# Kernel tuning notes

Hardware: AMD Instinct MI355X
Metric: run time of the kernel (lower is better)

## Reference

```python
import jax, jax.numpy as jnp
import numpy as np

N_GT, N_NODES, N_SPECIES, N_EDGES, D, L = 512, 399, 200, 397, 64, 2


def setup_inputs() -> dict:
    rng = np.random.default_rng(0)
    # Random recursive trees: parent of node i is uniform in [0, i).
    par = (rng.random((N_GT, N_NODES - 1)) * np.arange(1, N_NODES)).astype(np.int64)
    child = np.broadcast_to(np.arange(1, N_NODES), (N_GT, N_NODES - 1))
    off = (np.arange(N_GT, dtype=np.int64) * N_NODES)[:, None]
    c = (child + off).ravel()
    p = (par + off).ravel()
    # Both directions, as in the original [2, 2E_gt] convention.
    edge_index = np.stack([np.concatenate([c, p]), np.concatenate([p, c])])
    sp = np.full(N_NODES, -1, dtype=np.int64)
    sp[:N_SPECIES] = np.arange(N_SPECIES)
    sp_ids = np.tile(sp, N_GT)
    leaf_mask = sp_ids >= 0
    batch_vec = np.repeat(np.arange(N_GT, dtype=np.int64), N_NODES)
    # Clades: random species subsets per species-tree edge, guaranteed nonempty.
    pe = rng.uniform(0.05, 0.5, (N_EDGES, 1))
    clade_mask = rng.random((N_EDGES, N_SPECIES)) < pe
    clade_mask[np.arange(N_EDGES), rng.integers(0, N_SPECIES, N_EDGES)] = True
    key = jax.random.key(0)
    ks = jax.random.split(key, 3)
    s = 1.0 / np.sqrt(D)
    return {
        "edge_index": jnp.asarray(edge_index),
        "sp_ids": jnp.asarray(sp_ids),
        "leaf_mask": jnp.asarray(leaf_mask),
        "batch_vec": jnp.asarray(batch_vec),
        "clade_mask": jnp.asarray(clade_mask),
        "n_gt": N_GT,
        "emb_table": jax.random.normal(ks[0], (N_SPECIES + 1, D), jnp.float32),
        "W1": jax.random.normal(ks[1], (L, D, D), jnp.float32) * s,
        "b1": jnp.zeros((L, D), jnp.float32),
        "W2": jax.random.normal(ks[2], (L, D, D), jnp.float32) * s,
        "b2": jnp.zeros((L, D), jnp.float32),
        "eps": jnp.zeros((L,), jnp.float32),  # GINConv train_eps init 0
        "ln_gamma": jnp.ones((L, D), jnp.float32),
        "ln_beta": jnp.zeros((L, D), jnp.float32),
    }


def _layernorm(x, g, b):
    mu = x.mean(-1, keepdims=True)
    var = ((x - mu) ** 2).mean(-1, keepdims=True)
    return (x - mu) * jax.lax.rsqrt(var + 1e-5) * g + b


def reference(edge_index, sp_ids, leaf_mask, batch_vec, clade_mask, n_gt,
              emb_table, W1, b1, W2, b2, eps, ln_gamma, ln_beta):
    n_nodes = sp_ids.shape[0]
    n_edges, n_species = clade_mask.shape
    d = emb_table.shape[1]
    # Species embedding (internal nodes -> extra row n_species).
    emb_ids = jnp.where(sp_ids < 0, n_species, sp_ids)
    x = emb_table[emb_ids]  # [Nn, D]
    src, dst = edge_index[0], edge_index[1]
    for l in range(W1.shape[0]):
        # GINConv: mlp((1+eps)*x + sum_neighbors x_j), residual, LayerNorm.
        msg = jax.ops.segment_sum(x[src], dst, num_segments=n_nodes)
        h = (1.0 + eps[l]) * x + msg
        h = jax.nn.relu(h @ W1[l] + b1[l]) @ W2[l] + b2[l]
        x = _layernorm(x + h, ln_gamma[l], ln_beta[l])
        # dropout is identity in eval mode
    # Species pooling: mean over valid leaves per (gene tree, species).
    w = (leaf_mask & (sp_ids >= 0)).astype(x.dtype)  # [Nn]
    comp = batch_vec * n_species + jnp.maximum(sp_ids, 0)
    pool_size = n_gt * n_species
    sums = jax.ops.segment_sum(x * w[:, None], comp, num_segments=pool_size)
    cnts = jax.ops.segment_sum(w, comp, num_segments=pool_size)
    pool = (sums / jnp.maximum(cnts, 1.0)[:, None]).reshape(n_gt, n_species, d)
    valid = (cnts > 0).astype(x.dtype).reshape(n_gt, n_species)  # [G, S]
    # Clade pooling per species-tree edge (vectorized over the per-edge loop).
    mf = clade_mask.astype(x.dtype)  # [E, S]
    csum = jnp.einsum('es,gsd->egd', mf, pool * valid[:, :, None])  # [E,G,D]
    ccnt = mf @ valid.T  # [E, G] valid-species count per (edge, gene tree)
    gt_means = csum / jnp.maximum(ccnt, 1.0)[:, :, None]
    has = (ccnt > 0).astype(x.dtype)  # gene trees with data for this edge
    n_v = has.sum(1)  # [E]
    mean = (gt_means * has[:, :, None]).sum(1) / jnp.maximum(n_v, 1.0)[:, None]
    diff = (gt_means - mean[:, None, :]) * has[:, :, None]
    var = (diff ** 2).sum(1) / jnp.maximum(n_v - 1.0, 1.0)[:, None]  # unbiased
    ok = (n_v > 1)[:, None]
    std = jnp.where(ok, jnp.sqrt(jnp.where(ok, var, 1.0)), 0.0)
    mean = jnp.where((n_v > 0)[:, None], mean, 0.0)
    return jnp.concatenate([mean, std], axis=-1)  # [n_edges, 2*D]
```

## Files before the change

### kernel.cpp

```cpp
#include <hip/hip_runtime.h>

#define SMAX 200
#define NPG 399

typedef __bf16 bf16x8 __attribute__((ext_vector_type(8)));
typedef _Float16 half8 __attribute__((ext_vector_type(8)));
typedef float f32x4 __attribute__((ext_vector_type(4)));

__device__ __forceinline__ unsigned short f2bf(float f) {
  unsigned u = __float_as_uint(f);
  unsigned r = (u + 0x7FFFu + ((u >> 16) & 1u)) >> 16;
  return (unsigned short)r;
}
__device__ __forceinline__ int xel(int node, int dim) {
  return node * 64 + ((((dim >> 3)) ^ (node & 7)) << 3) + (dim & 7);
}

__global__ __launch_bounds__(256) void k_prep(const int* __restrict__ clade,
                                              unsigned short* __restrict__ mfA,
                                              unsigned* __restrict__ mfbits,
                                              int n_edges, int n_species) {
  int stride = gridDim.x * 256;
  for (int idx = blockIdx.x * 256 + threadIdx.x; idx < 25 * 7 * 512;
       idx += stride) {
    int fi = idx >> 9, within = idx & 511;
    int mt = fi / 7, kt = fi % 7;
    int l = within >> 3, j = within & 7;
    int e = mt * 16 + (l & 15);
    int s = kt * 32 + ((l >> 4) & 3) * 8 + j;
    unsigned short v = 0;
    if (e < n_edges && s < n_species && clade[(size_t)e * n_species + s] != 0)
      v = 0x3F80;
    mfA[idx] = v;
  }
  for (int idx = blockIdx.x * 256 + threadIdx.x; idx < 400 * 8; idx += stride) {
    int e = idx >> 3, w = idx & 7;
    unsigned bits = 0;
    if (e < n_edges && w < 7) {
      for (int b = 0; b < 32; ++b) {
        int s = w * 32 + b;
        if (s < n_species && clade[(size_t)e * n_species + s] != 0)
          bits |= 1u << b;
      }
    }
    mfbits[idx] = bits;
  }
}

__global__ __launch_bounds__(512) void k_tree(
    const float* __restrict__ emb, const int* __restrict__ sp,
    const int* __restrict__ leaf, const int* __restrict__ src,
    const int* __restrict__ dst, const float* __restrict__ W1,
    const float* __restrict__ b1, const float* __restrict__ W2,
    const float* __restrict__ b2, const float* __restrict__ eps_p,
    const float* __restrict__ gam, const float* __restrict__ bet,
    const unsigned short* __restrict__ mfA, const unsigned* __restrict__ mfbits,
    _Float16* __restrict__ gmat, float* __restrict__ has, int npg,
    int n_species, int n_edges, int n_gt) {
  __shared__ __attribute__((aligned(16))) _Float16 sA[NPG * 64];
  __shared__ __attribute__((aligned(16))) _Float16 sB[NPG * 64];
  __shared__ __attribute__((aligned(16))) _Float16 sWf[2][2][4096];
  __shared__ __attribute__((aligned(16))) _Float16 sT[8][1024];
  __shared__ int sStart[NPG + 1];
  __shared__ int sChild[NPG - 1];
  __shared__ int sPar[NPG];
  __shared__ int sCnt[NPG];

  int g = blockIdx.x, tid = threadIdx.x;
  int base = g * npg, nEt = npg - 1, ebase = g * nEt;
  int w = tid >> 6, lane = tid & 63;
  int cc = lane & 15, gq = lane >> 4;

  for (int i = tid; i < npg + 1; i += 512) sStart[i] = 0;
  for (int i = tid; i < npg; i += 512) sCnt[i] = 0;
  __syncthreads();
  for (int idx = tid; idx < 4096; idx += 512) {
    int k = idx >> 6, n = idx & 63;
    int frag = (k >> 5) * 4 + (n >> 4);
    int ln = ((k >> 3) & 3) * 16 + (n & 15);
    int j = k & 7;
    int o = frag * 512 + ln * 8 + j;
    sWf[0][0][o] = (_Float16)W1[idx];
    sWf[0][1][o] = (_Float16)W2[idx];
    sWf[1][0][o] = (_Float16)W1[4096 + idx];
    sWf[1][1][o] = (_Float16)W2[4096 + idx];
  }
  for (int idx = tid; idx < npg * 8; idx += 512) {
    int node = idx >> 3, ch = idx & 7;
    int s = sp[base + node];
    int row = (s < 0) ? n_species : s;
    float4 v0 = reinterpret_cast<const float4*>(emb)[row * 16 + ch * 2];
    float4 v1 = reinterpret_cast<const float4*>(emb)[row * 16 + ch * 2 + 1];
    half8 h;
    h[0] = (_Float16)v0.x; h[1] = (_Float16)v0.y;
    h[2] = (_Float16)v0.z; h[3] = (_Float16)v0.w;
    h[4] = (_Float16)v1.x; h[5] = (_Float16)v1.y;
    h[6] = (_Float16)v1.z; h[7] = (_Float16)v1.w;
    *reinterpret_cast<half8*>(&sA[node * 64 + ((ch ^ (node & 7)) << 3)]) = h;
  }
  for (int i = tid; i < nEt; i += 512) {
    int c = src[ebase + i] - base;
    int p = dst[ebase + i] - base;
    sPar[c] = p;
    atomicAdd(&sStart[p + 1], 1);
  }
  __syncthreads();
  if (w == 0) {
    int run = 0;
    for (int chunk = 0; chunk * 64 < npg + 1; ++chunk) {
      int idx = chunk * 64 + lane;
      int v = (idx < npg + 1) ? sStart[idx] : 0;
      for (int off = 1; off < 64; off <<= 1) {
        int t2 = __shfl_up(v, off);
        if (lane >= off) v += t2;
      }
      v += run;
      if (idx < npg + 1) sStart[idx] = v;
      run = __shfl(v, 63);
    }
  }
  __syncthreads();
  for (int c = tid + 1; c < npg; c += 512) {
    int p = sPar[c];
    int pos = sStart[p] + atomicAdd(&sCnt[p], 1);
    sChild[pos] = c;
  }
  __syncthreads();

  _Float16* tb = sT[w];
  int t0w = w * 3;
  int t1w = (w == 7) ? 25 : t0w + 3;
  for (int l = 0; l < 2; ++l) {
    const _Float16* xin = l ? sB : sA;
    _Float16* xout = l ? sA : sB;
    const half8* xin8 = reinterpret_cast<const half8*>(xin);
    float e1 = 1.0f + eps_p[l];
    float b1v[4], b2v[4], gv[4], bv[4];
#pragma unroll
    for (int nt = 0; nt < 4; ++nt) {
      b1v[nt] = b1[l * 64 + cc + 16 * nt];
      b2v[nt] = b2[l * 64 + cc + 16 * nt];
      gv[nt] = gam[l * 64 + cc + 16 * nt];
      bv[nt] = bet[l * 64 + cc + 16 * nt];
    }
    const half8* B1 = reinterpret_cast<const half8*>(sWf[l][0]);
    const half8* B2 = reinterpret_cast<const half8*>(sWf[l][1]);
    for (int t = t0w; t < t1w; ++t) {
      int n0 = t * 16;
      int node = n0 + cc;
      bool vn = node < npg;
      int nd2 = vn ? node : 0;
      int j0v = vn ? sStart[nd2] : 0;
      int cnt = vn ? (sStart[nd2 + 1] - j0v) : 0;
      half8 s0 = xin8[nd2 * 8 + (gq ^ (nd2 & 7))];
      half8 s1 = xin8[nd2 * 8 + ((4 + gq) ^ (nd2 & 7))];
      bool hasp = vn && node > 0;
      int pr = hasp ? sPar[nd2] : 0;
      half8 p0 = xin8[pr * 8 + (gq ^ (pr & 7))];
      half8 p1 = xin8[pr * 8 + ((4 + gq) ^ (pr & 7))];
      float a0f[8], a1f[8];
#pragma unroll
      for (int d = 0; d < 8; ++d) {
        a0f[d] = e1 * (float)s0[d] + (hasp ? (float)p0[d] : 0.f);
        a1f[d] = e1 * (float)s1[d] + (hasp ? (float)p1[d] : 0.f);
      }
      int cmax = cnt;
#pragma unroll
      for (int off = 1; off < 64; off <<= 1)
        cmax = max(cmax, __shfl_xor(cmax, off));
      cmax = __builtin_amdgcn_readfirstlane(cmax);
#pragma unroll 2
      for (int k = 0; k < cmax; ++k) {
        bool act = k < cnt;
        int jidx = act ? (j0v + k) : 0;
        int c = sChild[jidx];
        half8 v0 = xin8[c * 8 + (gq ^ (c & 7))];
        half8 v1 = xin8[c * 8 + ((4 + gq) ^ (c & 7))];
        if (act) {
#pragma unroll
          for (int d = 0; d < 8; ++d) {
            a0f[d] += (float)v0[d];
            a1f[d] += (float)v1[d];
          }
        }
      }
      half8 a0, a1;
#pragma unroll
      for (int d = 0; d < 8; ++d) {
        a0[d] = (_Float16)a0f[d];
        a1[d] = (_Float16)a1f[d];
      }
      f32x4 tacc[4];
#pragma unroll
      for (int nt = 0; nt < 4; ++nt) tacc[nt] = (f32x4){0.f, 0.f, 0.f, 0.f};
#pragma unroll
      for (int nt = 0; nt < 4; ++nt) {
        tacc[nt] = __builtin_amdgcn_mfma_f32_16x16x32_f16(
            a0, B1[nt * 64 + lane], tacc[nt], 0, 0, 0);
        tacc[nt] = __builtin_amdgcn_mfma_f32_16x16x32_f16(
            a1, B1[(4 + nt) * 64 + lane], tacc[nt], 0, 0, 0);
      }
#pragma unroll
      for (int nt = 0; nt < 4; ++nt)
#pragma unroll
        for (int r = 0; r < 4; ++r) {
          int m = gq * 4 + r;
          tb[m * 64 + ((cc + 16 * nt) ^ ((m & 7) << 3))] =
              (_Float16)fmaxf(tacc[nt][r] + b1v[nt], 0.f);
        }
      int sw = (cc & 7) << 3;
      half8 c0 =
          *reinterpret_cast<const half8*>(&tb[cc * 64 + ((gq * 8) ^ sw)]);
      half8 c1 =
          *reinterpret_cast<const half8*>(&tb[cc * 64 + ((32 + gq * 8) ^ sw)]);
      f32x4 hacc[4];
#pragma unroll
      for (int nt = 0; nt < 4; ++nt) hacc[nt] = (f32x4){0.f, 0.f, 0.f, 0.f};
#pragma unroll
      for (int nt = 0; nt < 4; ++nt) {
        hacc[nt] = __builtin_amdgcn_mfma_f32_16x16x32_f16(
            c0, B2[nt * 64 + lane], hacc[nt], 0, 0, 0);
        hacc[nt] = __builtin_amdgcn_mfma_f32_16x16x32_f16(
            c1, B2[(4 + nt) * 64 + lane], hacc[nt], 0, 0, 0);
      }
      float y[4][4];
#pragma unroll
      for (int r = 0; r < 4; ++r) {
        int nd3 = n0 + gq * 4 + r;
        bool v3 = nd3 < npg;
        int nds = v3 ? nd3 : 0;
#pragma unroll
        for (int nt = 0; nt < 4; ++nt) {
          float xv = (float)xin[xel(nds, cc + 16 * nt)];
          y[r][nt] = (v3 ? xv : 0.f) + hacc[nt][r] + b2v[nt];
        }
      }
#pragma unroll
      for (int r = 0; r < 4; ++r) {
        float s = y[r][0] + y[r][1] + y[r][2] + y[r][3];
        s += __shfl_xor(s, 1);
        s += __shfl_xor(s, 2);
        s += __shfl_xor(s, 4);
        s += __shfl_xor(s, 8);
        float mu = s * (1.f / 64.f);
        float d0 = y[r][0] - mu, d1 = y[r][1] - mu;
        float d2 = y[r][2] - mu, d3 = y[r][3] - mu;
        float v = d0 * d0 + d1 * d1 + d2 * d2 + d3 * d3;
        v += __shfl_xor(v, 1);
        v += __shfl_xor(v, 2);
        v += __shfl_xor(v, 4);
        v += __shfl_xor(v, 8);
        float iv = rsqrtf(v * (1.f / 64.f) + 1e-5f);
        int nd3 = n0 + gq * 4 + r;
        if (nd3 < npg) {
#pragma unroll
          for (int nt = 0; nt < 4; ++nt)
            xout[xel(nd3, cc + 16 * nt)] =
                (_Float16)((y[r][nt] - mu) * iv * gv[nt] + bv[nt]);
        }
      }
    }
    __syncthreads();
  }

  unsigned short* sBfU = reinterpret_cast<unsigned short*>(&sWf[0][0][0]);
  char* aux = reinterpret_cast<char*>(&sT[0][0]);
  float* sInv = reinterpret_cast<float*>(aux);
  float* sHas = reinterpret_cast<float*>(aux + 1600);
  unsigned* svb = reinterpret_cast<unsigned*>(aux + 3200);
  for (int i = tid; i < n_species + 1; i += 512) sStart[i] = 0;
  for (int i = tid; i < n_species; i += 512) sCnt[i] = 0;
  {
    float4 z4 = {0.f, 0.f, 0.f, 0.f};
    for (int i = tid; i < 1792; i += 512)
      reinterpret_cast<float4*>(sBfU)[i] = z4;
  }
  __syncthreads();
  for (int i = tid; i < npg; i += 512) {
    int s = sp[base + i];
    if (s >= 0 && leaf[base + i] != 0) atomicAdd(&sStart[s + 1], 1);
  }
  __syncthreads();
  if (w == 0) {
    int run = 0;
    for (int chunk = 0; chunk * 64 < n_species + 1; ++chunk) {
      int idx = chunk * 64 + lane;
      int v = (idx < n_species + 1) ? sStart[idx] : 0;
      for (int off = 1; off < 64; off <<= 1) {
        int t2 = __shfl_up(v, off);
        if (lane >= off) v += t2;
      }
      v += run;
      if (idx < n_species + 1) sStart[idx] = v;
      run = __shfl(v, 63);
    }
  }
  __syncthreads();
  for (int i = tid; i < npg; i += 512) {
    int s = sp[base + i];
    if (s >= 0 && leaf[base + i] != 0) {
      int pos = sStart[s] + atomicAdd(&sCnt[s], 1);
      sPar[pos] = i;
    }
  }
  __syncthreads();
  for (int idx = tid; idx < n_species * 8; idx += 512) {
    int s = idx >> 3, dc = idx & 7;
    int j0 = sStart[s], j1 = sStart[s + 1];
    float sum[8] = {0.f, 0.f, 0.f, 0.f, 0.f, 0.f, 0.f, 0.f};
    for (int j2 = j0; j2 < j1; ++j2) {
      int nd = sPar[j2];
      half8 v = *reinterpret_cast<const half8*>(
          &sA[nd * 64 + ((dc ^ (nd & 7)) << 3)]);
#pragma unroll
      for (int dd = 0; dd < 8; ++dd) sum[dd] += (float)v[dd];
    }
    float invc = (j1 > j0) ? 1.f / (float)(j1 - j0) : 0.f;
#pragma unroll
    for (int dd = 0; dd < 8; ++dd) {
      int d = dc * 8 + dd;
      int frag = (s >> 5) * 4 + (d >> 4);
      int ln = ((s >> 3) & 3) * 16 + (d & 15);
      sBfU[frag * 512 + ln * 8 + (s & 7)] = f2bf(sum[dd] * invc);
    }
  }
  if (tid < 7) {
    unsigned bits = 0;
    for (int b = 0; b < 32; ++b) {
      int s = tid * 32 + b;
      if (s < n_species && sStart[s + 1] > sStart[s]) bits |= 1u << b;
    }
    svb[tid] = bits;
  }
  __syncthreads();
  for (int e = tid; e < 400; e += 512) {
    unsigned ccv = 0;
#pragma unroll
    for (int w2 = 0; w2 < 7; ++w2) ccv += __popc(mfbits[e * 8 + w2] & svb[w2]);
    sInv[e] = 1.f / (float)max(ccv, 1u);
    sHas[e] = (ccv > 0) ? 1.f : 0.f;
  }
  __syncthreads();
  const bf16x8* A = reinterpret_cast<const bf16x8*>(mfA);
  const bf16x8* Bb = reinterpret_cast<const bf16x8*>(sBfU);
  for (int mt = w; mt < 25; mt += 8) {
    bf16x8 af[7];
#pragma unroll
    for (int kt = 0; kt < 7; ++kt) af[kt] = A[(mt * 7 + kt) * 64 + lane];
    f32x4 acc0 = {0.f, 0.f, 0.f, 0.f};
    f32x4 acc1 = {0.f, 0.f, 0.f, 0.f};
    f32x4 acc2 = {0.f, 0.f, 0.f, 0.f};
    f32x4 acc3 = {0.f, 0.f, 0.f, 0.f};
#pragma unroll
    for (int kt = 0; kt < 7; ++kt) {
      const bf16x8* B = Bb + kt * 256 + lane;
      acc0 = __builtin_amdgcn_mfma_f32_16x16x32_bf16(af[kt], B[0], acc0, 0, 0, 0);
      acc1 = __builtin_amdgcn_mfma_f32_16x16x32_bf16(af[kt], B[64], acc1, 0, 0, 0);
      acc2 = __builtin_amdgcn_mfma_f32_16x16x32_bf16(af[kt], B[128], acc2, 0, 0, 0);
      acc3 = __builtin_amdgcn_mfma_f32_16x16x32_bf16(af[kt], B[192], acc3, 0, 0, 0);
    }
    int rbase = mt * 16 + (lane >> 4) * 4;
    int col = lane & 15;
#pragma unroll
    for (int r = 0; r < 4; ++r) {
      int e = rbase + r;
      if (e >= n_edges) continue;
      float inv = sInv[e];
      _Float16* gp = gmat + ((size_t)e * n_gt + g) * 64 + col;
      gp[0] = (_Float16)(acc0[r] * inv);
      gp[16] = (_Float16)(acc1[r] * inv);
      gp[32] = (_Float16)(acc2[r] * inv);
      gp[48] = (_Float16)(acc3[r] * inv);
      if (col == 0) has[(size_t)e * n_gt + g] = sHas[e];
    }
  }
}

__global__ __launch_bounds__(512) void k_stat(const _Float16* __restrict__ gmat,
                                              const float* __restrict__ has,
                                              float* __restrict__ out,
                                              int n_gt) {
  __shared__ float red1[8][64];
  __shared__ float red2[8][64];
  __shared__ float redn[8];
  int e = blockIdx.x;
  int tid = threadIdx.x, w = tid >> 6, lane = tid & 63;
  const _Float16* ge = gmat + (size_t)e * n_gt * 64;
  const float* he = has + (size_t)e * n_gt;
  float S1 = 0.f, S2 = 0.f, nv = 0.f;
  for (int g = w; g < n_gt; g += 8) {
    float h = he[g];
    float v = (float)ge[g * 64 + lane];
    S1 += h * v;
    S2 += h * v * v;
    nv += h;
  }
  red1[w][lane] = S1;
  red2[w][lane] = S2;
  if (lane == 0) redn[w] = nv;
  __syncthreads();
  if (w == 0) {
    float s1 = 0.f, s2 = 0.f, n_v = 0.f;
#pragma unroll
    for (int j = 0; j < 8; ++j) {
      s1 += red1[j][lane];
      s2 += red2[j][lane];
      n_v += redn[j];
    }
    float mean = s1 / fmaxf(n_v, 1.f);
    float var = (s2 - s1 * s1 / fmaxf(n_v, 1.f)) / fmaxf(n_v - 1.f, 1.f);
    float stdv = (n_v > 1.f) ? sqrtf(fmaxf(var, 0.f)) : 0.f;
    out[(size_t)e * 128 + lane] = (n_v > 0.f) ? mean : 0.f;
    out[(size_t)e * 128 + 64 + lane] = stdv;
  }
}

extern "C" void kernel_launch(void* const* d_in, const int* in_sizes, int n_in,
                              void* d_out, int out_size, void* d_ws, size_t ws_size,
                              hipStream_t stream) {
  (void)n_in; (void)out_size; (void)ws_size;
  const int* edge_index = (const int*)d_in[0];
  const int* sp_ids = (const int*)d_in[1];
  const int* leaf_mask = (const int*)d_in[2];
  const int* clade_mask = (const int*)d_in[4];
  const float* emb = (const float*)d_in[6];
  const float* W1 = (const float*)d_in[7];
  const float* b1 = (const float*)d_in[8];
  const float* W2 = (const float*)d_in[9];
  const float* b2 = (const float*)d_in[10];
  const float* eps = (const float*)d_in[11];
  const float* lng = (const float*)d_in[12];
  const float* lnb = (const float*)d_in[13];
  float* out = (float*)d_out;

  const int n_nodes = in_sizes[1];
  const int nE = in_sizes[0] / 2;
  const int n_species = in_sizes[6] / 64 - 1;
  const int n_edges = in_sizes[4] / n_species;
  const int n_gt = 512;
  const int npg = n_nodes / n_gt;

  const int* src = edge_index;
  const int* dst = edge_index + nE;

  _Float16* gmat = (_Float16*)d_ws;
  size_t gsz =
      ((size_t)n_edges * n_gt * 64 * sizeof(_Float16) + 255ul) & ~255ul;
  float* has = (float*)((char*)d_ws + gsz);
  size_t hsz = ((size_t)n_edges * n_gt * sizeof(float) + 255ul) & ~255ul;
  unsigned short* mfA = (unsigned short*)((char*)d_ws + gsz + hsz);
  size_t masz = ((size_t)25 * 7 * 512 * sizeof(unsigned short) + 255ul) & ~255ul;
  unsigned* mfbits = (unsigned*)((char*)d_ws + gsz + hsz + masz);

  k_prep<<<64, 256, 0, stream>>>(clade_mask, mfA, mfbits, n_edges, n_species);
  k_tree<<<n_gt, 512, 0, stream>>>(emb, sp_ids, leaf_mask, src, dst, W1, b1,
                                   W2, b2, eps, lng, lnb, mfA, mfbits, gmat,
                                   has, npg, n_species, n_edges, n_gt);
  k_stat<<<n_edges, 512, 0, stream>>>(gmat, has, out, n_gt);
}
```

Before: 123.0 us.

## Widen tree kernel to 12 waves and split edge statistics reduction across blocks

The per-gene-tree kernel now runs 768 threads (12 waves) instead of 512, spreading the 25 node tiles and the clade-pool matmul tiles over more waves. To fit the extra per-wave scratch in shared memory, weights are staged one layer at a time, with an extra barrier per layer. The statistics kernel is split into four partial-sum blocks per edge plus a small finalize kernel. This is meant to raise parallelism, at the cost of an extra launch, more shared memory and register pressure under the higher launch bound, and uneven tile counts per wave.

```diff
diff --git a/kernel.cpp b/kernel.cpp
--- a/kernel.cpp
+++ b/kernel.cpp
@@ -47,7 +47,7 @@
   }
 }
 
-__global__ __launch_bounds__(512) void k_tree(
+__global__ __launch_bounds__(768) void k_tree(
     const float* __restrict__ emb, const int* __restrict__ sp,
     const int* __restrict__ leaf, const int* __restrict__ src,
     const int* __restrict__ dst, const float* __restrict__ W1,
@@ -59,8 +59,8 @@
     int n_species, int n_edges, int n_gt) {
   __shared__ __attribute__((aligned(16))) _Float16 sA[NPG * 64];
   __shared__ __attribute__((aligned(16))) _Float16 sB[NPG * 64];
-  __shared__ __attribute__((aligned(16))) _Float16 sWf[2][2][4096];
-  __shared__ __attribute__((aligned(16))) _Float16 sT[8][1024];
+  __shared__ __attribute__((aligned(16))) _Float16 sWf[2][4096];
+  __shared__ __attribute__((aligned(16))) _Float16 sT[14][1024];
   __shared__ int sStart[NPG + 1];
   __shared__ int sChild[NPG - 1];
   __shared__ int sPar[NPG];
@@ -71,21 +71,10 @@
   int w = tid >> 6, lane = tid & 63;
   int cc = lane & 15, gq = lane >> 4;
 
-  for (int i = tid; i < npg + 1; i += 512) sStart[i] = 0;
-  for (int i = tid; i < npg; i += 512) sCnt[i] = 0;
-  __syncthreads();
-  for (int idx = tid; idx < 4096; idx += 512) {
-    int k = idx >> 6, n = idx & 63;
-    int frag = (k >> 5) * 4 + (n >> 4);
-    int ln = ((k >> 3) & 3) * 16 + (n & 15);
-    int j = k & 7;
-    int o = frag * 512 + ln * 8 + j;
-    sWf[0][0][o] = (_Float16)W1[idx];
-    sWf[0][1][o] = (_Float16)W2[idx];
-    sWf[1][0][o] = (_Float16)W1[4096 + idx];
-    sWf[1][1][o] = (_Float16)W2[4096 + idx];
-  }
-  for (int idx = tid; idx < npg * 8; idx += 512) {
+  for (int i = tid; i < npg + 1; i += 768) sStart[i] = 0;
+  for (int i = tid; i < npg; i += 768) sCnt[i] = 0;
+  __syncthreads();
+  for (int idx = tid; idx < npg * 8; idx += 768) {
     int node = idx >> 3, ch = idx & 7;
     int s = sp[base + node];
     int row = (s < 0) ? n_species : s;
@@ -98,7 +87,7 @@
     h[6] = (_Float16)v1.z; h[7] = (_Float16)v1.w;
     *reinterpret_cast<half8*>(&sA[node * 64 + ((ch ^ (node & 7)) << 3)]) = h;
   }
-  for (int i = tid; i < nEt; i += 512) {
+  for (int i = tid; i < nEt; i += 768) {
     int c = src[ebase + i] - base;
     int p = dst[ebase + i] - base;
     sPar[c] = p;
@@ -120,7 +109,7 @@
     }
   }
   __syncthreads();
-  for (int c = tid + 1; c < npg; c += 512) {
+  for (int c = tid + 1; c < npg; c += 768) {
     int p = sPar[c];
     int pos = sStart[p] + atomicAdd(&sCnt[p], 1);
     sChild[pos] = c;
@@ -128,9 +117,19 @@
   __syncthreads();
 
   _Float16* tb = sT[w];
-  int t0w = w * 3;
-  int t1w = (w == 7) ? 25 : t0w + 3;
+  int t0w = (w * 25) / 12;
+  int t1w = ((w + 1) * 25) / 12;
   for (int l = 0; l < 2; ++l) {
+    for (int idx = tid; idx < 4096; idx += 768) {
+      int k = idx >> 6, n = idx & 63;
+      int frag = (k >> 5) * 4 + (n >> 4);
+      int ln = ((k >> 3) & 3) * 16 + (n & 15);
+      int j = k & 7;
+      int o = frag * 512 + ln * 8 + j;
+      sWf[0][o] = (_Float16)W1[l * 4096 + idx];
+      sWf[1][o] = (_Float16)W2[l * 4096 + idx];
+    }
+    __syncthreads();
     const _Float16* xin = l ? sB : sA;
     _Float16* xout = l ? sA : sB;
     const half8* xin8 = reinterpret_cast<const half8*>(xin);
@@ -143,8 +142,8 @@
       gv[nt] = gam[l * 64 + cc + 16 * nt];
       bv[nt] = bet[l * 64 + cc + 16 * nt];
     }
-    const half8* B1 = reinterpret_cast<const half8*>(sWf[l][0]);
-    const half8* B2 = reinterpret_cast<const half8*>(sWf[l][1]);
+    const half8* B1 = reinterpret_cast<const half8*>(sWf[0]);
+    const half8* B2 = reinterpret_cast<const half8*>(sWf[1]);
     for (int t = t0w; t < t1w; ++t) {
       int n0 = t * 16;
       int node = n0 + cc;
@@ -263,20 +262,20 @@
     __syncthreads();
   }
 
-  unsigned short* sBfU = reinterpret_cast<unsigned short*>(&sWf[0][0][0]);
-  char* aux = reinterpret_cast<char*>(&sT[0][0]);
+  unsigned short* sBfU = reinterpret_cast<unsigned short*>(&sT[0][0]);
+  char* aux = reinterpret_cast<char*>(&sWf[0][0]);
   float* sInv = reinterpret_cast<float*>(aux);
   float* sHas = reinterpret_cast<float*>(aux + 1600);
   unsigned* svb = reinterpret_cast<unsigned*>(aux + 3200);
-  for (int i = tid; i < n_species + 1; i += 512) sStart[i] = 0;
-  for (int i = tid; i < n_species; i += 512) sCnt[i] = 0;
+  for (int i = tid; i < n_species + 1; i += 768) sStart[i] = 0;
+  for (int i = tid; i < n_species; i += 768) sCnt[i] = 0;
   {
     float4 z4 = {0.f, 0.f, 0.f, 0.f};
-    for (int i = tid; i < 1792; i += 512)
+    for (int i = tid; i < 1792; i += 768)
       reinterpret_cast<float4*>(sBfU)[i] = z4;
   }
   __syncthreads();
-  for (int i = tid; i < npg; i += 512) {
+  for (int i = tid; i < npg; i += 768) {
     int s = sp[base + i];
     if (s >= 0 && leaf[base + i] != 0) atomicAdd(&sStart[s + 1], 1);
   }
@@ -296,7 +295,7 @@
     }
   }
   __syncthreads();
-  for (int i = tid; i < npg; i += 512) {
+  for (int i = tid; i < npg; i += 768) {
     int s = sp[base + i];
     if (s >= 0 && leaf[base + i] != 0) {
       int pos = sStart[s] + atomicAdd(&sCnt[s], 1);
@@ -304,7 +303,7 @@
     }
   }
   __syncthreads();
-  for (int idx = tid; idx < n_species * 8; idx += 512) {
+  for (int idx = tid; idx < n_species * 8; idx += 768) {
     int s = idx >> 3, dc = idx & 7;
     int j0 = sStart[s], j1 = sStart[s + 1];
     float sum[8] = {0.f, 0.f, 0.f, 0.f, 0.f, 0.f, 0.f, 0.f};
@@ -333,7 +332,7 @@
     svb[tid] = bits;
   }
   __syncthreads();
-  for (int e = tid; e < 400; e += 512) {
+  for (int e = tid; e < 400; e += 768) {
     unsigned ccv = 0;
 #pragma unroll
     for (int w2 = 0; w2 < 7; ++w2) ccv += __popc(mfbits[e * 8 + w2] & svb[w2]);
@@ -343,7 +342,7 @@
   __syncthreads();
   const bf16x8* A = reinterpret_cast<const bf16x8*>(mfA);
   const bf16x8* Bb = reinterpret_cast<const bf16x8*>(sBfU);
-  for (int mt = w; mt < 25; mt += 8) {
+  for (int mt = w; mt < 25; mt += 12) {
     bf16x8 af[7];
 #pragma unroll
     for (int kt = 0; kt < 7; ++kt) af[kt] = A[(mt * 7 + kt) * 64 + lane];
@@ -376,21 +375,22 @@
   }
 }
 
-__global__ __launch_bounds__(512) void k_stat(const _Float16* __restrict__ gmat,
-                                              const float* __restrict__ has,
-                                              float* __restrict__ out,
-                                              int n_gt) {
-  __shared__ float red1[8][64];
-  __shared__ float red2[8][64];
-  __shared__ float redn[8];
-  int e = blockIdx.x;
+__global__ __launch_bounds__(256) void k_stat2(const _Float16* __restrict__ gmat,
+                                               const float* __restrict__ has,
+                                               float* __restrict__ part,
+                                               int n_gt) {
+  __shared__ float red1[4][64];
+  __shared__ float red2[4][64];
+  __shared__ float redn[4];
+  int b = blockIdx.x;
+  int e = b >> 2, q = b & 3;
   int tid = threadIdx.x, w = tid >> 6, lane = tid & 63;
-  const _Float16* ge = gmat + (size_t)e * n_gt * 64;
-  const float* he = has + (size_t)e * n_gt;
+  const _Float16* ge = gmat + ((size_t)e * n_gt + q * 128) * 64;
+  const float* he = has + (size_t)e * n_gt + q * 128;
   float S1 = 0.f, S2 = 0.f, nv = 0.f;
-  for (int g = w; g < n_gt; g += 8) {
-    float h = he[g];
-    float v = (float)ge[g * 64 + lane];
+  for (int i = w; i < 128; i += 4) {
+    float h = he[i];
+    float v = (float)ge[i * 64 + lane];
     S1 += h * v;
     S2 += h * v * v;
     nv += h;
@@ -402,17 +402,35 @@
   if (w == 0) {
     float s1 = 0.f, s2 = 0.f, n_v = 0.f;
 #pragma unroll
-    for (int j = 0; j < 8; ++j) {
+    for (int j = 0; j < 4; ++j) {
       s1 += red1[j][lane];
       s2 += red2[j][lane];
       n_v += redn[j];
     }
-    float mean = s1 / fmaxf(n_v, 1.f);
-    float var = (s2 - s1 * s1 / fmaxf(n_v, 1.f)) / fmaxf(n_v - 1.f, 1.f);
-    float stdv = (n_v > 1.f) ? sqrtf(fmaxf(var, 0.f)) : 0.f;
-    out[(size_t)e * 128 + lane] = (n_v > 0.f) ? mean : 0.f;
-    out[(size_t)e * 128 + 64 + lane] = stdv;
-  }
+    float* p = part + (size_t)b * 130;
+    p[lane] = s1;
+    p[64 + lane] = s2;
+    if (lane == 0) p[128] = n_v;
+  }
+}
+
+__global__ __launch_bounds__(64) void k_fin(const float* __restrict__ part,
+                                            float* __restrict__ out) {
+  int e = blockIdx.x;
+  int lane = threadIdx.x;
+  float s1 = 0.f, s2 = 0.f, n_v = 0.f;
+#pragma unroll
+  for (int q = 0; q < 4; ++q) {
+    const float* p = part + (size_t)(e * 4 + q) * 130;
+    s1 += p[lane];
+    s2 += p[64 + lane];
+    n_v += p[128];
+  }
+  float mean = s1 / fmaxf(n_v, 1.f);
+  float var = (s2 - s1 * s1 / fmaxf(n_v, 1.f)) / fmaxf(n_v - 1.f, 1.f);
+  float stdv = (n_v > 1.f) ? sqrtf(fmaxf(var, 0.f)) : 0.f;
+  out[(size_t)e * 128 + lane] = (n_v > 0.f) ? mean : 0.f;
+  out[(size_t)e * 128 + 64 + lane] = stdv;
 }
 
 extern "C" void kernel_launch(void* const* d_in, const int* in_sizes, int n_in,
@@ -451,10 +469,13 @@
   unsigned short* mfA = (unsigned short*)((char*)d_ws + gsz + hsz);
   size_t masz = ((size_t)25 * 7 * 512 * sizeof(unsigned short) + 255ul) & ~255ul;
   unsigned* mfbits = (unsigned*)((char*)d_ws + gsz + hsz + masz);
+  size_t mbsz = ((size_t)400 * 8 * sizeof(unsigned) + 255ul) & ~255ul;
+  float* part = (float*)((char*)d_ws + gsz + hsz + masz + mbsz);
 
   k_prep<<<64, 256, 0, stream>>>(clade_mask, mfA, mfbits, n_edges, n_species);
-  k_tree<<<n_gt, 512, 0, stream>>>(emb, sp_ids, leaf_mask, src, dst, W1, b1,
+  k_tree<<<n_gt, 768, 0, stream>>>(emb, sp_ids, leaf_mask, src, dst, W1, b1,
                                    W2, b2, eps, lng, lnb, mfA, mfbits, gmat,
                                    has, npg, n_species, n_edges, n_gt);
-  k_stat<<<n_edges, 512, 0, stream>>>(gmat, has, out, n_gt);
-}
+  k_stat2<<<n_edges * 4, 256, 0, stream>>>(gmat, has, part, n_gt);
+  k_fin<<<n_edges, 64, 0, stream>>>(part, out);
+}
```

Result: slower. 131.0 us (+6.5%).

## Split per-edge stats reduction across four blocks and batch child gathers

Applied to the files above, without the earlier changes.

The child-aggregation loop in the tree kernel now loads four child indices and their feature vectors before accumulating, so more shared-memory loads are in flight at once. The per-edge statistics kernel is split into four blocks per species edge, each covering 128 gene trees and writing partial sums to workspace. A new small kernel then combines the partials into the mean and std. The aim is more parallelism on the GPU for the reduction stage, at the cost of an extra launch and a partials buffer.

```diff
diff --git a/kernel.cpp b/kernel.cpp
--- a/kernel.cpp
+++ b/kernel.cpp
@@ -169,18 +169,28 @@
       for (int off = 1; off < 64; off <<= 1)
         cmax = max(cmax, __shfl_xor(cmax, off));
       cmax = __builtin_amdgcn_readfirstlane(cmax);
-#pragma unroll 2
-      for (int k = 0; k < cmax; ++k) {
-        bool act = k < cnt;
-        int jidx = act ? (j0v + k) : 0;
-        int c = sChild[jidx];
-        half8 v0 = xin8[c * 8 + (gq ^ (c & 7))];
-        half8 v1 = xin8[c * 8 + ((4 + gq) ^ (c & 7))];
-        if (act) {
-#pragma unroll
-          for (int d = 0; d < 8; ++d) {
-            a0f[d] += (float)v0[d];
-            a1f[d] += (float)v1[d];
+      for (int k0 = 0; k0 < cmax; k0 += 4) {
+        int ci[4];
+#pragma unroll
+        for (int jj = 0; jj < 4; ++jj) {
+          int kk = k0 + jj;
+          ci[jj] = sChild[(kk < cnt) ? (j0v + kk) : 0];
+        }
+        half8 v0[4], v1[4];
+#pragma unroll
+        for (int jj = 0; jj < 4; ++jj) {
+          int c = ci[jj];
+          v0[jj] = xin8[c * 8 + (gq ^ (c & 7))];
+          v1[jj] = xin8[c * 8 + ((4 + gq) ^ (c & 7))];
+        }
+#pragma unroll
+        for (int jj = 0; jj < 4; ++jj) {
+          if (k0 + jj < cnt) {
+#pragma unroll
+            for (int d = 0; d < 8; ++d) {
+              a0f[d] += (float)v0[jj][d];
+              a1f[d] += (float)v1[jj][d];
+            }
           }
         }
       }
@@ -376,21 +386,22 @@
   }
 }
 
-__global__ __launch_bounds__(512) void k_stat(const _Float16* __restrict__ gmat,
-                                              const float* __restrict__ has,
-                                              float* __restrict__ out,
-                                              int n_gt) {
-  __shared__ float red1[8][64];
-  __shared__ float red2[8][64];
-  __shared__ float redn[8];
-  int e = blockIdx.x;
+__global__ __launch_bounds__(256) void k_stat2(const _Float16* __restrict__ gmat,
+                                               const float* __restrict__ has,
+                                               float* __restrict__ part,
+                                               int n_gt) {
+  __shared__ float red1[4][64];
+  __shared__ float red2[4][64];
+  __shared__ float redn[4];
+  int b = blockIdx.x;
+  int e = b >> 2, q = b & 3;
   int tid = threadIdx.x, w = tid >> 6, lane = tid & 63;
-  const _Float16* ge = gmat + (size_t)e * n_gt * 64;
-  const float* he = has + (size_t)e * n_gt;
+  const _Float16* ge = gmat + ((size_t)e * n_gt + q * 128) * 64;
+  const float* he = has + (size_t)e * n_gt + q * 128;
   float S1 = 0.f, S2 = 0.f, nv = 0.f;
-  for (int g = w; g < n_gt; g += 8) {
-    float h = he[g];
-    float v = (float)ge[g * 64 + lane];
+  for (int i = w; i < 128; i += 4) {
+    float h = he[i];
+    float v = (float)ge[i * 64 + lane];
     S1 += h * v;
     S2 += h * v * v;
     nv += h;
@@ -402,17 +413,35 @@
   if (w == 0) {
     float s1 = 0.f, s2 = 0.f, n_v = 0.f;
 #pragma unroll
-    for (int j = 0; j < 8; ++j) {
+    for (int j = 0; j < 4; ++j) {
       s1 += red1[j][lane];
       s2 += red2[j][lane];
       n_v += redn[j];
     }
-    float mean = s1 / fmaxf(n_v, 1.f);
-    float var = (s2 - s1 * s1 / fmaxf(n_v, 1.f)) / fmaxf(n_v - 1.f, 1.f);
-    float stdv = (n_v > 1.f) ? sqrtf(fmaxf(var, 0.f)) : 0.f;
-    out[(size_t)e * 128 + lane] = (n_v > 0.f) ? mean : 0.f;
-    out[(size_t)e * 128 + 64 + lane] = stdv;
-  }
+    float* p = part + (size_t)b * 130;
+    p[lane] = s1;
+    p[64 + lane] = s2;
+    if (lane == 0) p[128] = n_v;
+  }
+}
+
+__global__ __launch_bounds__(64) void k_fin(const float* __restrict__ part,
+                                            float* __restrict__ out) {
+  int e = blockIdx.x;
+  int lane = threadIdx.x;
+  float s1 = 0.f, s2 = 0.f, n_v = 0.f;
+#pragma unroll
+  for (int q = 0; q < 4; ++q) {
+    const float* p = part + (size_t)(e * 4 + q) * 130;
+    s1 += p[lane];
+    s2 += p[64 + lane];
+    n_v += p[128];
+  }
+  float mean = s1 / fmaxf(n_v, 1.f);
+  float var = (s2 - s1 * s1 / fmaxf(n_v, 1.f)) / fmaxf(n_v - 1.f, 1.f);
+  float stdv = (n_v > 1.f) ? sqrtf(fmaxf(var, 0.f)) : 0.f;
+  out[(size_t)e * 128 + lane] = (n_v > 0.f) ? mean : 0.f;
+  out[(size_t)e * 128 + 64 + lane] = stdv;
 }
 
 extern "C" void kernel_launch(void* const* d_in, const int* in_sizes, int n_in,
@@ -451,10 +480,13 @@
   unsigned short* mfA = (unsigned short*)((char*)d_ws + gsz + hsz);
   size_t masz = ((size_t)25 * 7 * 512 * sizeof(unsigned short) + 255ul) & ~255ul;
   unsigned* mfbits = (unsigned*)((char*)d_ws + gsz + hsz + masz);
+  size_t mbsz = ((size_t)400 * 8 * sizeof(unsigned) + 255ul) & ~255ul;
+  float* part = (float*)((char*)d_ws + gsz + hsz + masz + mbsz);
 
   k_prep<<<64, 256, 0, stream>>>(clade_mask, mfA, mfbits, n_edges, n_species);
   k_tree<<<n_gt, 512, 0, stream>>>(emb, sp_ids, leaf_mask, src, dst, W1, b1,
                                    W2, b2, eps, lng, lnb, mfA, mfbits, gmat,
                                    has, npg, n_species, n_edges, n_gt);
-  k_stat<<<n_edges, 512, 0, stream>>>(gmat, has, out, n_gt);
-}
+  k_stat2<<<n_edges * 4, 256, 0, stream>>>(gmat, has, part, n_gt);
+  k_fin<<<n_edges, 64, 0, stream>>>(part, out);
+}
```

After: 116.9 us. 1.05x faster.
